# Optimization experiments

Measured on AMD Instinct MI355X. Metric: run time of the kernel, lower is better.

## Reference

```python
import jax, jax.numpy as jnp
import numpy as np

B, T, H, Q = 64, 2048, 512, 512


def setup_inputs() -> dict:
    key = jax.random.key(0)
    k1, k2, k3, k4, k5 = jax.random.split(key, 5)
    query = jax.random.normal(k1, (B, Q), dtype=jnp.float32)
    encoder_outputs = jax.random.normal(k2, (B, T, H), dtype=jnp.float32)
    # nn.Linear(hidden_size, query_size): weight [Q, H], bias [Q]
    W = jax.random.normal(k3, (Q, H), dtype=jnp.float32) * (1.0 / np.sqrt(H))
    b = jax.random.normal(k4, (Q,), dtype=jnp.float32) * 0.01
    tgt_index = jax.random.randint(k5, (B,), 0, T, dtype=jnp.int64)
    return {"query": query, "encoder_outputs": encoder_outputs, "W": W, "b": b,
            "tgt_index": tgt_index}


def reference(query, encoder_outputs, W, b, tgt_index):
    # method == 'general': energy[b,i] = (W @ enc[b,i] + bias) . query[b]
    proj = jnp.einsum('bth,qh->btq', encoder_outputs, W) + b       # [B,T,Q]
    energies = jnp.einsum('btq,bq->bt', proj, query)               # [B,T]
    # ragged mask: position i valid iff i <= tgt_index[b] (this_len = tgt_index+1)
    mask = jnp.arange(T)[None, :] <= tgt_index[:, None]            # [B,T]
    logits = jnp.where(mask, energies, -jnp.inf)
    attn = jax.nn.softmax(logits, axis=-1)                         # [B,T]
    context = jnp.einsum('bt,bth->bh', attn, encoder_outputs)      # [B,H]
    return context
```

## Files before the change

kernel.cpp:

```cpp
#include <hip/hip_runtime.h>
#include <hip/hip_bf16.h>
#include <math.h>


#define B 64
#define T 2048
#define H 512
#define Q 512
#define TT 128
#define NCH (T / TT)
#define NPW (NCH * 4)

__global__ void k_proj(const float* __restrict__ query,
                       const float* __restrict__ W,
                       const float* __restrict__ bias,
                       float* __restrict__ v,
                       float* __restrict__ c) {
    int b = blockIdx.y;
    int tid = threadIdx.x;
    int h = blockIdx.x * 128 + tid;

    __shared__ float sq[Q];
    for (int i = tid; i < Q; i += 128) sq[i] = query[(size_t)b * Q + i];
    __syncthreads();

    float acc = 0.0f;
#pragma unroll 8
    for (int q = 0; q < Q; ++q) acc += sq[q] * W[(size_t)q * H + h];
    v[(size_t)b * H + h] = acc;

    if (blockIdx.x == 0) {
        float pb = 0.0f;
        for (int i = tid; i < Q; i += 128) pb += sq[i] * bias[i];
        for (int off = 32; off; off >>= 1) pb += __shfl_xor(pb, off, 64);
        __shared__ float sred[2];
        if ((tid & 63) == 0) sred[tid >> 6] = pb;
        __syncthreads();
        if (tid == 0) c[b] = sred[0] + sred[1];
    }
}

__global__ __launch_bounds__(256) void k_attn(const float* __restrict__ enc,
                                              const float* __restrict__ v,
                                              const float* __restrict__ c,
                                              const int* __restrict__ tgt,
                                              float* __restrict__ pm,
                                              float* __restrict__ pl,
                                              float* __restrict__ pctx) {
    int b = blockIdx.y;
    int len = tgt[b] + 1;
    int t0 = blockIdx.x * TT;
    if (t0 >= len) return;
    int n = min(TT, len - t0);

    __shared__ float sv[H];
    int tid = threadIdx.x;
    sv[tid]       = v[(size_t)b * H + tid];
    sv[tid + 256] = v[(size_t)b * H + 256 + tid];
    __syncthreads();

    int wave = tid >> 6;
    int lane = tid & 63;
    const float4* sv4 = (const float4*)sv;
    float4 w0 = sv4[lane];
    float4 w1 = sv4[lane + 64];
    float cb = c[b];

    float m = -INFINITY, l = 0.0f;
    float4 a0 = {0.f, 0.f, 0.f, 0.f};
    float4 a1 = {0.f, 0.f, 0.f, 0.f};

    for (int t = wave; t < n; t += 4) {
        const float4* row = (const float4*)(enc + ((size_t)b * T + t0 + t) * H);
        float4 x0 = row[lane];
        float4 x1 = row[lane + 64];
        float e = x0.x * w0.x + x0.y * w0.y + x0.z * w0.z + x0.w * w0.w
                + x1.x * w1.x + x1.y * w1.y + x1.z * w1.z + x1.w * w1.w;
        for (int off = 32; off; off >>= 1) e += __shfl_xor(e, off, 64);
        e += cb;

        float mn = fmaxf(m, e);
        float alpha = __expf(m - mn);
        float p = __expf(e - mn);
        l = l * alpha + p;
        a0.x = a0.x * alpha + p * x0.x;
        a0.y = a0.y * alpha + p * x0.y;
        a0.z = a0.z * alpha + p * x0.z;
        a0.w = a0.w * alpha + p * x0.w;
        a1.x = a1.x * alpha + p * x1.x;
        a1.y = a1.y * alpha + p * x1.y;
        a1.z = a1.z * alpha + p * x1.z;
        a1.w = a1.w * alpha + p * x1.w;
        m = mn;
    }

    int pidx = (b * NCH + blockIdx.x) * 4 + wave;
    if (lane == 0) { pm[pidx] = m; pl[pidx] = l; }
    float4* dst = (float4*)(pctx + (size_t)pidx * H);
    dst[lane]      = a0;
    dst[lane + 64] = a1;
}

__global__ void k_combine(const float* __restrict__ pm,
                          const float* __restrict__ pl,
                          const float* __restrict__ pctx,
                          const int* __restrict__ tgt,
                          float* __restrict__ out) {
    int b = blockIdx.x;
    int len = tgt[b] + 1;
    int nch = (len + TT - 1) / TT;
    int np = nch * 4;
    int base = b * NPW;
    int tid = threadIdx.x;

    float M = -INFINITY;
    for (int j = 0; j < np; ++j) M = fmaxf(M, pm[base + j]);
    float L = 0.0f;
    for (int j = 0; j < np; ++j) L += pl[base + j] * __expf(pm[base + j] - M);
    float invL = 1.0f / L;

    float acc0 = 0.0f, acc1 = 0.0f;
    for (int j = 0; j < np; ++j) {
        float mj = pm[base + j];
        float w = (mj == -INFINITY) ? 0.0f : __expf(mj - M) * invL;
        const float2* pc = (const float2*)(pctx + (size_t)(base + j) * H);
        float2 x = pc[tid];
        acc0 += w * x.x;
        acc1 += w * x.y;
    }
    out[(size_t)b * H + 2 * tid]     = acc0;
    out[(size_t)b * H + 2 * tid + 1] = acc1;
}

extern "C" void kernel_launch(void* const* d_in, const int* in_sizes, int n_in,
                              void* d_out, int out_size, void* d_ws, size_t ws_size,
                              hipStream_t stream) {
    const float* query = (const float*)d_in[0];
    const float* enc   = (const float*)d_in[1];
    const float* W     = (const float*)d_in[2];
    const float* bias  = (const float*)d_in[3];
    const int*   tgt   = (const int*)d_in[4];
    float* out = (float*)d_out;

    char* ws = (char*)d_ws;
    float* v    = (float*)ws;  ws += (size_t)B * H * sizeof(float);
    float* c    = (float*)ws;  ws += 256;
    float* pm   = (float*)ws;  ws += (size_t)B * NPW * sizeof(float);
    float* pl   = (float*)ws;  ws += (size_t)B * NPW * sizeof(float);
    float* pctx = (float*)ws;

    k_proj<<<dim3(H / 128, B), dim3(128), 0, stream>>>(query, W, bias, v, c);
    k_attn<<<dim3(NCH, B), dim3(256), 0, stream>>>(enc, v, c, tgt, pm, pl, pctx);
    k_combine<<<dim3(B), dim3(256), 0, stream>>>(pm, pl, pctx, tgt, out);
}
```

Measured before the change: 392.3 us.

## Halve attention chunk size and process two rows per wave iteration

Chunk size TT drops from 128 to 64, which doubles the number of blocks in the attention kernel. Each wave now loads two encoder rows per iteration and keeps two independent online-softmax states, merging them at the end. This raises memory-level parallelism and shortens the serial dependency chain. The shared-memory staging of v is replaced with direct global loads, and the combine kernel guards against empty partials. In exchange there are twice as many partial results to write and reduce, and more registers are used.

```diff
diff --git a/kernel.cpp b/kernel.cpp
--- a/kernel.cpp
+++ b/kernel.cpp
@@ -7,7 +7,7 @@
 #define T 2048
 #define H 512
 #define Q 512
-#define TT 128
+#define TT 64
 #define NCH (T / TT)
 #define NPW (NCH * 4)
 
@@ -53,49 +53,80 @@
     if (t0 >= len) return;
     int n = min(TT, len - t0);
 
-    __shared__ float sv[H];
     int tid = threadIdx.x;
-    sv[tid]       = v[(size_t)b * H + tid];
-    sv[tid + 256] = v[(size_t)b * H + 256 + tid];
-    __syncthreads();
-
     int wave = tid >> 6;
     int lane = tid & 63;
-    const float4* sv4 = (const float4*)sv;
-    float4 w0 = sv4[lane];
-    float4 w1 = sv4[lane + 64];
+
+    const float4* v4 = (const float4*)(v + (size_t)b * H);
+    float4 w0 = v4[lane];
+    float4 w1 = v4[lane + 64];
     float cb = c[b];
 
-    float m = -INFINITY, l = 0.0f;
-    float4 a0 = {0.f, 0.f, 0.f, 0.f};
-    float4 a1 = {0.f, 0.f, 0.f, 0.f};
+    float mA = -INFINITY, lA = 0.0f;
+    float mB = -INFINITY, lB = 0.0f;
+    float4 a0 = {0.f,0.f,0.f,0.f}, a1 = {0.f,0.f,0.f,0.f};
+    float4 b0 = {0.f,0.f,0.f,0.f}, b1 = {0.f,0.f,0.f,0.f};
 
-    for (int t = wave; t < n; t += 4) {
-        const float4* row = (const float4*)(enc + ((size_t)b * T + t0 + t) * H);
-        float4 x0 = row[lane];
-        float4 x1 = row[lane + 64];
-        float e = x0.x * w0.x + x0.y * w0.y + x0.z * w0.z + x0.w * w0.w
-                + x1.x * w1.x + x1.y * w1.y + x1.z * w1.z + x1.w * w1.w;
-        for (int off = 32; off; off >>= 1) e += __shfl_xor(e, off, 64);
-        e += cb;
+    const float* encb = enc + (size_t)b * T * H;
 
-        float mn = fmaxf(m, e);
-        float alpha = __expf(m - mn);
-        float p = __expf(e - mn);
-        l = l * alpha + p;
-        a0.x = a0.x * alpha + p * x0.x;
-        a0.y = a0.y * alpha + p * x0.y;
-        a0.z = a0.z * alpha + p * x0.z;
-        a0.w = a0.w * alpha + p * x0.w;
-        a1.x = a1.x * alpha + p * x1.x;
-        a1.y = a1.y * alpha + p * x1.y;
-        a1.z = a1.z * alpha + p * x1.z;
-        a1.w = a1.w * alpha + p * x1.w;
-        m = mn;
+    for (int t = wave; t < n; t += 8) {
+        const float4* rowA = (const float4*)(encb + (size_t)(t0 + t) * H);
+        float4 xa0 = rowA[lane];
+        float4 xa1 = rowA[lane + 64];
+        bool hasB = (t + 4) < n;
+        float4 xb0 = {0.f,0.f,0.f,0.f}, xb1 = {0.f,0.f,0.f,0.f};
+        if (hasB) {
+            const float4* rowB = (const float4*)(encb + (size_t)(t0 + t + 4) * H);
+            xb0 = rowB[lane];
+            xb1 = rowB[lane + 64];
+        }
+
+        float eA = xa0.x*w0.x + xa0.y*w0.y + xa0.z*w0.z + xa0.w*w0.w
+                 + xa1.x*w1.x + xa1.y*w1.y + xa1.z*w1.z + xa1.w*w1.w;
+        float eB = xb0.x*w0.x + xb0.y*w0.y + xb0.z*w0.z + xb0.w*w0.w
+                 + xb1.x*w1.x + xb1.y*w1.y + xb1.z*w1.z + xb1.w*w1.w;
+        for (int off = 32; off; off >>= 1) {
+            eA += __shfl_xor(eA, off, 64);
+            eB += __shfl_xor(eB, off, 64);
+        }
+        eA += cb;
+        eB += cb;
+
+        {
+            float mn = fmaxf(mA, eA);
+            float alpha = __expf(mA - mn);
+            float p = __expf(eA - mn);
+            lA = lA * alpha + p;
+            a0.x = a0.x*alpha + p*xa0.x;  a0.y = a0.y*alpha + p*xa0.y;
+            a0.z = a0.z*alpha + p*xa0.z;  a0.w = a0.w*alpha + p*xa0.w;
+            a1.x = a1.x*alpha + p*xa1.x;  a1.y = a1.y*alpha + p*xa1.y;
+            a1.z = a1.z*alpha + p*xa1.z;  a1.w = a1.w*alpha + p*xa1.w;
+            mA = mn;
+        }
+        if (hasB) {
+            float mn = fmaxf(mB, eB);
+            float alpha = __expf(mB - mn);
+            float p = __expf(eB - mn);
+            lB = lB * alpha + p;
+            b0.x = b0.x*alpha + p*xb0.x;  b0.y = b0.y*alpha + p*xb0.y;
+            b0.z = b0.z*alpha + p*xb0.z;  b0.w = b0.w*alpha + p*xb0.w;
+            b1.x = b1.x*alpha + p*xb1.x;  b1.y = b1.y*alpha + p*xb1.y;
+            b1.z = b1.z*alpha + p*xb1.z;  b1.w = b1.w*alpha + p*xb1.w;
+            mB = mn;
+        }
     }
 
+    float mn = fmaxf(mA, mB);
+    float aAl = (mA == -INFINITY) ? 0.0f : __expf(mA - mn);
+    float aBl = (mB == -INFINITY) ? 0.0f : __expf(mB - mn);
+    float lT = lA * aAl + lB * aBl;
+    a0.x = a0.x*aAl + b0.x*aBl;  a0.y = a0.y*aAl + b0.y*aBl;
+    a0.z = a0.z*aAl + b0.z*aBl;  a0.w = a0.w*aAl + b0.w*aBl;
+    a1.x = a1.x*aAl + b1.x*aBl;  a1.y = a1.y*aAl + b1.y*aBl;
+    a1.z = a1.z*aAl + b1.z*aBl;  a1.w = a1.w*aAl + b1.w*aBl;
+
     int pidx = (b * NCH + blockIdx.x) * 4 + wave;
-    if (lane == 0) { pm[pidx] = m; pl[pidx] = l; }
+    if (lane == 0) { pm[pidx] = mn; pl[pidx] = lT; }
     float4* dst = (float4*)(pctx + (size_t)pidx * H);
     dst[lane]      = a0;
     dst[lane + 64] = a1;
@@ -116,7 +147,10 @@
     float M = -INFINITY;
     for (int j = 0; j < np; ++j) M = fmaxf(M, pm[base + j]);
     float L = 0.0f;
-    for (int j = 0; j < np; ++j) L += pl[base + j] * __expf(pm[base + j] - M);
+    for (int j = 0; j < np; ++j) {
+        float mj = pm[base + j];
+        if (mj != -INFINITY) L += pl[base + j] * __expf(mj - M);
+    }
     float invL = 1.0f / L;
 
     float acc0 = 0.0f, acc1 = 0.0f;
```

Measured after the change: 420.8 us. 1.07x slower.

## Process four rows per wave iteration and merge wave partials in-block

Applied to the files above, without the earlier changes.

The attention kernel now has each wave load four encoder rows per iteration, interleaving their shuffle reductions and folding them into one online-softmax update with a single rescale. This raises memory-level parallelism and cuts per-row exp and shuffle latency. The four per-wave partial states are merged through shared memory inside the block, so one partial per chunk is written instead of four, which shrinks partial-context traffic and the combine kernel's loop. Out-of-range rows within a group of four are masked to -inf, but their loads still run unguarded, which may read past the valid length (still in bounds of the buffer except at the array end).

```diff
diff --git a/kernel.cpp b/kernel.cpp
--- a/kernel.cpp
+++ b/kernel.cpp
@@ -9,7 +9,6 @@
 #define Q 512
 #define TT 128
 #define NCH (T / TT)
-#define NPW (NCH * 4)
 
 __global__ void k_proj(const float* __restrict__ query,
                        const float* __restrict__ W,
@@ -53,52 +52,89 @@
     if (t0 >= len) return;
     int n = min(TT, len - t0);
 
-    __shared__ float sv[H];
     int tid = threadIdx.x;
-    sv[tid]       = v[(size_t)b * H + tid];
-    sv[tid + 256] = v[(size_t)b * H + 256 + tid];
-    __syncthreads();
-
     int wave = tid >> 6;
     int lane = tid & 63;
-    const float4* sv4 = (const float4*)sv;
-    float4 w0 = sv4[lane];
-    float4 w1 = sv4[lane + 64];
+
+    const float4* v4 = (const float4*)(v + (size_t)b * H);
+    float4 w0 = v4[lane];
+    float4 w1 = v4[lane + 64];
     float cb = c[b];
 
     float m = -INFINITY, l = 0.0f;
-    float4 a0 = {0.f, 0.f, 0.f, 0.f};
-    float4 a1 = {0.f, 0.f, 0.f, 0.f};
+    float4 a0 = {0.f,0.f,0.f,0.f}, a1 = {0.f,0.f,0.f,0.f};
+    const float* encb = enc + ((size_t)b * T + t0) * H;
 
-    for (int t = wave; t < n; t += 4) {
-        const float4* row = (const float4*)(enc + ((size_t)b * T + t0 + t) * H);
-        float4 x0 = row[lane];
-        float4 x1 = row[lane + 64];
-        float e = x0.x * w0.x + x0.y * w0.y + x0.z * w0.z + x0.w * w0.w
-                + x1.x * w1.x + x1.y * w1.y + x1.z * w1.z + x1.w * w1.w;
-        for (int off = 32; off; off >>= 1) e += __shfl_xor(e, off, 64);
-        e += cb;
+    for (int t = wave * 4; t < n; t += 16) {
+        const float4* r0 = (const float4*)(encb + (size_t)(t + 0) * H);
+        const float4* r1 = (const float4*)(encb + (size_t)(t + 1) * H);
+        const float4* r2 = (const float4*)(encb + (size_t)(t + 2) * H);
+        const float4* r3 = (const float4*)(encb + (size_t)(t + 3) * H);
+        float4 x00 = r0[lane], x01 = r0[lane + 64];
+        float4 x10 = r1[lane], x11 = r1[lane + 64];
+        float4 x20 = r2[lane], x21 = r2[lane + 64];
+        float4 x30 = r3[lane], x31 = r3[lane + 64];
 
-        float mn = fmaxf(m, e);
+        float e0 = x00.x*w0.x + x00.y*w0.y + x00.z*w0.z + x00.w*w0.w
+                 + x01.x*w1.x + x01.y*w1.y + x01.z*w1.z + x01.w*w1.w;
+        float e1 = x10.x*w0.x + x10.y*w0.y + x10.z*w0.z + x10.w*w0.w
+                 + x11.x*w1.x + x11.y*w1.y + x11.z*w1.z + x11.w*w1.w;
+        float e2 = x20.x*w0.x + x20.y*w0.y + x20.z*w0.z + x20.w*w0.w
+                 + x21.x*w1.x + x21.y*w1.y + x21.z*w1.z + x21.w*w1.w;
+        float e3 = x30.x*w0.x + x30.y*w0.y + x30.z*w0.z + x30.w*w0.w
+                 + x31.x*w1.x + x31.y*w1.y + x31.z*w1.z + x31.w*w1.w;
+
+        for (int off = 32; off; off >>= 1) {
+            e0 += __shfl_xor(e0, off, 64);
+            e1 += __shfl_xor(e1, off, 64);
+            e2 += __shfl_xor(e2, off, 64);
+            e3 += __shfl_xor(e3, off, 64);
+        }
+        e0 += cb;
+        e1 = (t + 1 < n) ? e1 + cb : -INFINITY;
+        e2 = (t + 2 < n) ? e2 + cb : -INFINITY;
+        e3 = (t + 3 < n) ? e3 + cb : -INFINITY;
+
+        float mn = fmaxf(fmaxf(fmaxf(e0, e1), fmaxf(e2, e3)), m);
         float alpha = __expf(m - mn);
-        float p = __expf(e - mn);
-        l = l * alpha + p;
-        a0.x = a0.x * alpha + p * x0.x;
-        a0.y = a0.y * alpha + p * x0.y;
-        a0.z = a0.z * alpha + p * x0.z;
-        a0.w = a0.w * alpha + p * x0.w;
-        a1.x = a1.x * alpha + p * x1.x;
-        a1.y = a1.y * alpha + p * x1.y;
-        a1.z = a1.z * alpha + p * x1.z;
-        a1.w = a1.w * alpha + p * x1.w;
+        float p0 = __expf(e0 - mn);
+        float p1 = __expf(e1 - mn);
+        float p2 = __expf(e2 - mn);
+        float p3 = __expf(e3 - mn);
+        l = l * alpha + (p0 + p1) + (p2 + p3);
+        a0.x = a0.x*alpha + p0*x00.x + p1*x10.x + p2*x20.x + p3*x30.x;
+        a0.y = a0.y*alpha + p0*x00.y + p1*x10.y + p2*x20.y + p3*x30.y;
+        a0.z = a0.z*alpha + p0*x00.z + p1*x10.z + p2*x20.z + p3*x30.z;
+        a0.w = a0.w*alpha + p0*x00.w + p1*x10.w + p2*x20.w + p3*x30.w;
+        a1.x = a1.x*alpha + p0*x01.x + p1*x11.x + p2*x21.x + p3*x31.x;
+        a1.y = a1.y*alpha + p0*x01.y + p1*x11.y + p2*x21.y + p3*x31.y;
+        a1.z = a1.z*alpha + p0*x01.z + p1*x11.z + p2*x21.z + p3*x31.z;
+        a1.w = a1.w*alpha + p0*x01.w + p1*x11.w + p2*x21.w + p3*x31.w;
         m = mn;
     }
 
-    int pidx = (b * NCH + blockIdx.x) * 4 + wave;
-    if (lane == 0) { pm[pidx] = m; pl[pidx] = l; }
-    float4* dst = (float4*)(pctx + (size_t)pidx * H);
-    dst[lane]      = a0;
-    dst[lane + 64] = a1;
+    __shared__ float sm4[4], sl4[4];
+    __shared__ float sctx[4 * H];
+    float4* sc = (float4*)(sctx + wave * H);
+    sc[lane]      = a0;
+    sc[lane + 64] = a1;
+    if (lane == 0) { sm4[wave] = m; sl4[wave] = l; }
+    __syncthreads();
+
+    float M = fmaxf(fmaxf(sm4[0], sm4[1]), fmaxf(sm4[2], sm4[3]));
+    float L = 0.0f, acc0 = 0.0f, acc1 = 0.0f;
+#pragma unroll
+    for (int j = 0; j < 4; ++j) {
+        float mj = sm4[j];
+        float wj = (mj == -INFINITY) ? 0.0f : __expf(mj - M);
+        L += sl4[j] * wj;
+        acc0 += wj * sctx[j * H + 2 * tid];
+        acc1 += wj * sctx[j * H + 2 * tid + 1];
+    }
+    int pidx = b * NCH + blockIdx.x;
+    if (tid == 0) { pm[pidx] = M; pl[pidx] = L; }
+    float2* dst = (float2*)(pctx + (size_t)pidx * H);
+    dst[tid] = make_float2(acc0, acc1);
 }
 
 __global__ void k_combine(const float* __restrict__ pm,
@@ -107,26 +143,29 @@
                           const int* __restrict__ tgt,
                           float* __restrict__ out) {
     int b = blockIdx.x;
+    int tid = threadIdx.x;
     int len = tgt[b] + 1;
     int nch = (len + TT - 1) / TT;
-    int np = nch * 4;
-    int base = b * NPW;
-    int tid = threadIdx.x;
+
+    __shared__ float spm[NCH], spl[NCH];
+    if (tid < nch) {
+        spm[tid] = pm[b * NCH + tid];
+        spl[tid] = pl[b * NCH + tid];
+    }
+    __syncthreads();
 
     float M = -INFINITY;
-    for (int j = 0; j < np; ++j) M = fmaxf(M, pm[base + j]);
+    for (int j = 0; j < nch; ++j) M = fmaxf(M, spm[j]);
     float L = 0.0f;
-    for (int j = 0; j < np; ++j) L += pl[base + j] * __expf(pm[base + j] - M);
+    for (int j = 0; j < nch; ++j) L += spl[j] * __expf(spm[j] - M);
     float invL = 1.0f / L;
 
     float acc0 = 0.0f, acc1 = 0.0f;
-    for (int j = 0; j < np; ++j) {
-        float mj = pm[base + j];
-        float w = (mj == -INFINITY) ? 0.0f : __expf(mj - M) * invL;
-        const float2* pc = (const float2*)(pctx + (size_t)(base + j) * H);
-        float2 x = pc[tid];
-        acc0 += w * x.x;
-        acc1 += w * x.y;
+    for (int j = 0; j < nch; ++j) {
+        float wj = __expf(spm[j] - M) * invL;
+        float2 x = ((const float2*)(pctx + (size_t)(b * NCH + j) * H))[tid];
+        acc0 += wj * x.x;
+        acc1 += wj * x.y;
     }
     out[(size_t)b * H + 2 * tid]     = acc0;
     out[(size_t)b * H + 2 * tid + 1] = acc1;
@@ -145,8 +184,8 @@
     char* ws = (char*)d_ws;
     float* v    = (float*)ws;  ws += (size_t)B * H * sizeof(float);
     float* c    = (float*)ws;  ws += 256;
-    float* pm   = (float*)ws;  ws += (size_t)B * NPW * sizeof(float);
-    float* pl   = (float*)ws;  ws += (size_t)B * NPW * sizeof(float);
+    float* pm   = (float*)ws;  ws += (size_t)B * NCH * sizeof(float);
+    float* pl   = (float*)ws;  ws += (size_t)B * NCH * sizeof(float);
     float* pctx = (float*)ws;
 
     k_proj<<<dim3(H / 128, B), dim3(128), 0, stream>>>(query, W, bias, v, c);
```

Measured after the change: 377.9 us. 3.7% less time.
